# Optimization experiments

Hardware: AMD Instinct MI355X
Metric: run time of the kernel (lower is better)

The kernel has to match this reference:

```python
import jax, jax.numpy as jnp
import numpy as np

RES = 512
MAX_DEPTH = 100.0
AMBIENT = 0.3
LIGHT_STREN = 0.8
SHININESS = 16.0
EPS = 1e-8


def _unit(v):
    return v / (jnp.linalg.norm(v, axis=-1, keepdims=True) + EPS)


def setup_inputs() -> dict:
    key = jax.random.key(0)
    ks = jax.random.split(key, 8)
    B, N, M, TEX = 1, 512, 128, 512
    verts = jax.random.uniform(ks[0], (B, N, 3), minval=-1.0, maxval=1.0, dtype=jnp.float32)
    faces = jax.random.randint(ks[1], (B, M, 3), 0, N, dtype=jnp.int32)
    normals = jax.random.normal(ks[2], (B, M, 3, 3), dtype=jnp.float32)
    uvs = jax.random.uniform(ks[3], (B, M, 3, 2), dtype=jnp.float32)
    textures = jax.random.uniform(ks[4], (B, TEX, TEX, 3), dtype=jnp.float32)
    f = RES / 2.0
    K = jnp.array([[f, 0.0, RES / 2.0], [0.0, f, RES / 2.0], [0.0, 0.0, 1.0]], jnp.float32)
    Ks = jnp.broadcast_to(K, (B, 3, 3))
    RT = jnp.concatenate([jnp.eye(3, dtype=jnp.float32), jnp.array([[0.0], [0.0], [2.0]], jnp.float32)], axis=1)
    RTs = jnp.broadcast_to(RT, (B, 3, 4))
    view_dir = jax.random.normal(ks[5], (B, 3), dtype=jnp.float32)
    light_dir = jax.random.normal(ks[6], (B, 3), dtype=jnp.float32)
    return {"verts": verts, "faces": faces, "normals": normals, "uvs": uvs,
            "textures": textures, "Ks": Ks, "RTs": RTs, "view_dir": view_dir, "light_dir": light_dir}


def _render(verts, faces, normals, uvs, textures, Ks, RTs, view_dir, light_dir):
    B = verts.shape[0]
    # camera space: cam = R @ v + t
    cam = jnp.einsum('bij,bnj->bni', RTs[:, :, :3], verts) + RTs[:, None, :, 3]
    # orthographic projection to pixel coords
    x = Ks[:, None, 0, 0] * cam[..., 0] + Ks[:, None, 0, 2]
    y = Ks[:, None, 1, 1] * cam[..., 1] + Ks[:, None, 1, 2]
    xy = jnp.stack([x, y], -1)            # [B,N,2]
    z = cam[..., 2]                        # [B,N]
    gather_v = jax.vmap(lambda a, f: a[f])
    tv = gather_v(xy, faces)               # [B,M,3,2] screen-space triangle corners
    tz = gather_v(z, faces)                # [B,M,3]
    # pixel centers, row-major (p = row*RES + col)
    ii = jnp.arange(RES, dtype=jnp.float32) + 0.5
    py, px = jnp.meshgrid(ii, ii, indexing='ij')
    pix = jnp.stack([px.ravel(), py.ravel()], -1)   # [P,2]

    def edge(a, b, p):
        return (b[..., 0] - a[..., 0]) * (p[..., 1] - a[..., 1]) - (b[..., 1] - a[..., 1]) * (p[..., 0] - a[..., 0])

    v0, v1, v2 = tv[:, None, :, 0], tv[:, None, :, 1], tv[:, None, :, 2]  # [B,1,M,2]
    p = pix[None, :, None]                                               # [1,P,1,2]
    w0 = edge(v1, v2, p)                   # [B,P,M]
    w1 = edge(v2, v0, p)
    w2 = edge(v0, v1, p)
    area = w0 + w1 + w2
    inside = (((w0 >= 0) & (w1 >= 0) & (w2 >= 0)) | ((w0 <= 0) & (w1 <= 0) & (w2 <= 0))) & (jnp.abs(area) > EPS)
    inv_a = 1.0 / jnp.where(jnp.abs(area) > EPS, area, 1.0)
    zpix = (w0 * tz[:, None, :, 0] + w1 * tz[:, None, :, 1] + w2 * tz[:, None, :, 2]) * inv_a
    valid = inside & (zpix > 0)
    zc = jnp.where(valid, zpix, MAX_DEPTH)   # [B,P,M] candidate depths
    depth = jnp.min(zc, axis=-1)             # z-buffer result [B,P]
    win = jnp.argmin(zc, axis=-1)             # winning triangle per pixel [B,P]
    hit = depth < MAX_DEPTH

    # recompute barycentrics for the winning triangle only (avoids [B,P,M,3])
    gpick = jax.vmap(lambda a, i: a[i])
    tvw = gpick(tv, win)                      # [B,P,3,2]
    nw = gpick(normals, win)                  # [B,P,3,3]
    uvw = gpick(uvs, win)                     # [B,P,3,2]
    pp = pix[None]                            # [1,P,2]

    def e2(a, b):
        return (b[..., 0] - a[..., 0]) * (pp[..., 1] - a[..., 1]) - (b[..., 1] - a[..., 1]) * (pp[..., 0] - a[..., 0])

    u0 = e2(tvw[:, :, 1], tvw[:, :, 2])
    u1 = e2(tvw[:, :, 2], tvw[:, :, 0])
    u2 = e2(tvw[:, :, 0], tvw[:, :, 1])
    ar = u0 + u1 + u2
    inv2 = 1.0 / jnp.where(jnp.abs(ar) > EPS, ar, 1.0)
    bary = jnp.stack([u0, u1, u2], -1) * inv2[..., None]   # [B,P,3]
    nrm = _unit(jnp.einsum('bpk,bpkc->bpc', bary, nw))     # interpolated normal
    uv = jnp.einsum('bpk,bpkc->bpc', bary, uvw)            # interpolated uv [B,P,2]

    # bilinear texture sampling
    Ht, Wt = textures.shape[1], textures.shape[2]
    uu = jnp.clip(uv[..., 0], 0.0, 1.0) * (Wt - 1)
    vv = jnp.clip(uv[..., 1], 0.0, 1.0) * (Ht - 1)
    x0 = jnp.floor(uu).astype(jnp.int32)
    y0 = jnp.floor(vv).astype(jnp.int32)
    x1 = jnp.minimum(x0 + 1, Wt - 1)
    y1 = jnp.minimum(y0 + 1, Ht - 1)
    fx = (uu - x0.astype(jnp.float32))[..., None]
    fy = (vv - y0.astype(jnp.float32))[..., None]
    tget = jax.vmap(lambda t, a, b: t[a, b])
    col = (tget(textures, y0, x0) * (1 - fx) * (1 - fy) + tget(textures, y0, x1) * fx * (1 - fy)
           + tget(textures, y1, x0) * (1 - fx) * fy + tget(textures, y1, x1) * fx * fy)  # [B,P,3]

    # Lambert diffuse + Blinn-Phong specular
    ld = _unit(light_dir)
    vd = _unit(view_dir)
    diff = jnp.clip(jnp.einsum('bpc,bc->bp', nrm, ld), 0.0)
    h = _unit(ld + vd)
    spec = LIGHT_STREN * jnp.clip(jnp.einsum('bpc,bc->bp', nrm, h), 0.0) ** SHININESS
    shade = col * (AMBIENT + LIGHT_STREN * diff)[..., None] + spec[..., None]
    rgb = jnp.where(hit[..., None], shade, 0.0)

    depths = depth.reshape(B, RES, RES)
    rgbs = rgb.reshape(B, RES, RES, 3)
    masks = hit.reshape(B, RES, RES).astype(jnp.int32)
    return depths, rgbs, masks


def reference(verts, faces, normals, uvs, textures, Ks, RTs, view_dir, light_dir):
    return _render(verts, faces, normals, uvs, textures, Ks, RTs, view_dir, light_dir)
```

## Files before the change

kernel.cpp:

```cpp
#include <hip/hip_runtime.h>
#include <math.h>

#pragma clang fp contract(off)

#define RES         512
#define TILE        16
#define TILESX      (RES / TILE)
#define MAXF        128
#define MAX_DEPTH   100.0f
#define AMBIENT     0.3f
#define LIGHT_STREN 0.8f
#define EPSF        1e-8f
#define MARG        1.0f
#define ZGUARD      1e-3f

__global__ __launch_bounds__(256) void mesh_render_tiled(
    const float* __restrict__ verts,
    const int*   __restrict__ faces,
    const float* __restrict__ normals,
    const float* __restrict__ uvs,
    const float* __restrict__ tex,
    const float* __restrict__ Ks,
    const float* __restrict__ RTs,
    const float* __restrict__ view_dir,
    const float* __restrict__ light_dir,
    float* __restrict__ out,
    int M, int TEXW, int TEXH)
{
    __shared__ float cfd[MAXF][16];
    __shared__ int   cid[MAXF];
    __shared__ int   scnt[2][8];
    __shared__ float slit[6];

    const int tid = threadIdx.x;
    const int tx  = blockIdx.x % TILESX;
    const int ty  = blockIdx.x / TILESX;
    const float PX0 = (float)(tx * TILE) + 0.5f;
    const float PY0 = (float)(ty * TILE) + 0.5f;

    bool flag = false;
    int  bkt  = -1;
    float e0dx=0,e0dy=0,e0ax=0,e0ay=0, e1dx=0,e1dy=0,e1ax=0,e1ay=0;
    float e2dx=0,e2dy=0,e2ax=0,e2ay=0, Z0=0,Z1=0,Z2=0, MZ=0;
    unsigned long long bmask = 0;

    if (tid < MAXF) {
        if (tid < M) {
            const float r00 = RTs[0], r01 = RTs[1], r02 = RTs[2],  t0 = RTs[3];
            const float r10 = RTs[4], r11 = RTs[5], r12 = RTs[6],  t1 = RTs[7];
            const float r20 = RTs[8], r21 = RTs[9], r22 = RTs[10], t2 = RTs[11];
            const float k00 = Ks[0], k02 = Ks[2], k11 = Ks[4], k12 = Ks[5];
            float X[3], Y[3], Z[3];
            #pragma unroll
            for (int k = 0; k < 3; ++k) {
                int vi = faces[tid * 3 + k];
                float vx = verts[vi * 3 + 0];
                float vy = verts[vi * 3 + 1];
                float vz = verts[vi * 3 + 2];
                float cx = ((r00 * vx + r01 * vy) + r02 * vz) + t0;
                float cy = ((r10 * vx + r11 * vy) + r12 * vz) + t1;
                float cz = ((r20 * vx + r21 * vy) + r22 * vz) + t2;
                X[k] = k00 * cx + k02;
                Y[k] = k11 * cy + k12;
                Z[k] = cz;
            }
            e0dx = X[2]-X[1]; e0dy = Y[2]-Y[1]; e0ax = X[1]; e0ay = Y[1];
            e1dx = X[0]-X[2]; e1dy = Y[0]-Y[2]; e1ax = X[2]; e1ay = Y[2];
            e2dx = X[1]-X[0]; e2dy = Y[1]-Y[0]; e2ax = X[0]; e2ay = Y[0];
            Z0 = Z[0]; Z1 = Z[1]; Z2 = Z[2];
            MZ = fminf(fminf(Z0, Z1), Z2);

            float minX = fminf(fminf(X[0],X[1]),X[2]);
            float maxX = fmaxf(fmaxf(X[0],X[1]),X[2]);
            float minY = fminf(fminf(Y[0],Y[1]),Y[2]);
            float maxY = fmaxf(fmaxf(Y[0],Y[1]),Y[2]);
            bool bb = (minX <= PX0 + 15.0f + MARG) && (maxX >= PX0 - MARG) &&
                      (minY <= PY0 + 15.0f + MARG) && (maxY >= PY0 - MARG);

            float wA0 = e0dx*(PY0-e0ay) - e0dy*(PX0-e0ax);
            float wA1 = e1dx*(PY0-e1ay) - e1dy*(PX0-e1ax);
            float wA2 = e2dx*(PY0-e2ay) - e2dy*(PX0-e2ax);
            float area = (wA0 + wA1) + wA2;
            float amin = fminf(area, 0.0f) - MARG, amax = fmaxf(area, 0.0f) + MARG;

            float s0x = -e0dy*15.0f, s0y = e0dx*15.0f;
            float s1x = -e1dy*15.0f, s1y = e1dx*15.0f;
            float s2x = -e2dy*15.0f, s2y = e2dx*15.0f;
            float t0min = wA0 + fminf(s0x,0.f) + fminf(s0y,0.f);
            float t0max = wA0 + fmaxf(s0x,0.f) + fmaxf(s0y,0.f);
            float t1min = wA1 + fminf(s1x,0.f) + fminf(s1y,0.f);
            float t1max = wA1 + fmaxf(s1x,0.f) + fmaxf(s1y,0.f);
            float t2min = wA2 + fminf(s2x,0.f) + fminf(s2y,0.f);
            float t2max = wA2 + fmaxf(s2x,0.f) + fmaxf(s2y,0.f);
            bool ok0 = (t0max >= amin) && (t0min <= amax);
            bool ok1 = (t1max >= amin) && (t1min <= amax);
            bool ok2 = (t2max >= amin) && (t2min <= amax);
            flag = bb && ok0 && ok1 && ok2;
            if (flag) {
                int bq = (int)((MZ - 1.0f) * 4.0f);
                bkt = bq < 0 ? 0 : (bq > 7 ? 7 : bq);
            }
        }
        #pragma unroll
        for (int k = 0; k < 8; ++k) {
            unsigned long long mk = __ballot(flag && (bkt == k));
            if (bkt == k) bmask = mk;
            if ((tid & 63) == 0) scnt[tid >> 6][k] = __popcll(mk);
        }
    }
    if (tid == 128) {
        float lx = light_dir[0], ly = light_dir[1], lz = light_dir[2];
        float ll = sqrtf((lx*lx + ly*ly) + lz*lz) + 1e-8f;
        lx /= ll; ly /= ll; lz /= ll;
        float vx = view_dir[0], vy = view_dir[1], vz = view_dir[2];
        float vl = sqrtf((vx*vx + vy*vy) + vz*vz) + 1e-8f;
        vx /= vl; vy /= vl; vz /= vl;
        float hx = lx + vx, hy = ly + vy, hz = lz + vz;
        float hl = sqrtf((hx*hx + hy*hy) + hz*hz) + 1e-8f;
        slit[0] = lx; slit[1] = ly; slit[2] = lz;
        slit[3] = hx / hl; slit[4] = hy / hl; slit[5] = hz / hl;
    }
    __syncthreads();

    if (flag) {
        int wv = tid >> 6;
        int base = 0;
        for (int k = 0; k < bkt; ++k) base += scnt[0][k] + scnt[1][k];
        if (wv == 1) base += scnt[0][bkt];
        int pos = base + __popcll(bmask & ((1ull << (tid & 63)) - 1ull));
        float* dd = cfd[pos];
        dd[0]=e0dx; dd[1]=e0dy; dd[2]=e0ax; dd[3]=e0ay;
        dd[4]=e1dx; dd[5]=e1dy; dd[6]=e1ax; dd[7]=e1ay;
        dd[8]=e2dx; dd[9]=e2dy; dd[10]=e2ax; dd[11]=e2ay;
        dd[12]=Z0;  dd[13]=Z1;  dd[14]=Z2;  dd[15]=MZ - ZGUARD;
        cid[pos] = tid;
    }
    __syncthreads();
    int cnt = 0;
    #pragma unroll
    for (int k = 0; k < 8; ++k) cnt += scnt[0][k] + scnt[1][k];

    const int lx_ = tid & (TILE-1), ly_ = tid / TILE;
    const float px = PX0 + (float)lx_;
    const float py = PY0 + (float)ly_;
    const int p = (ty*TILE + ly_) * RES + (tx*TILE + lx_);

    float best = MAX_DEPTH;
    float w0s = 0.0f, w1s = 0.0f, w2s = 0.0f, invs = 1.0f;
    int winpos = -1;
    for (int i = 0; i < cnt; ++i) {
        const float4 q3 = *reinterpret_cast<const float4*>(&cfd[i][12]);
        if (__all(q3.w >= best)) continue;
        const float4 q0 = *reinterpret_cast<const float4*>(&cfd[i][0]);
        const float4 q1 = *reinterpret_cast<const float4*>(&cfd[i][4]);
        const float4 q2 = *reinterpret_cast<const float4*>(&cfd[i][8]);
        float w0 = q0.x * (py - q0.w) - q0.y * (px - q0.z);
        float w1 = q1.x * (py - q1.w) - q1.y * (px - q1.z);
        float w2 = q2.x * (py - q2.w) - q2.y * (px - q2.z);
        float area = (w0 + w1) + w2;
        float mn = fminf(fminf(w0, w1), w2);
        float mx = fmaxf(fmaxf(w0, w1), w2);
        bool nz = fabsf(area) > EPSF;
        bool inside = ((mn >= 0.0f) || (mx <= 0.0f)) && nz;
        float inva = __builtin_amdgcn_rcpf(nz ? area : 1.0f);
        float zpix = ((w0 * q3.x + w1 * q3.y) + w2 * q3.z) * inva;
        float zc = (inside && (zpix > 0.0f)) ? zpix : MAX_DEPTH;
        if (zc < best) {
            best = zc; winpos = i;
            w0s = w0; w1s = w1; w2s = w2; invs = inva;
        }
    }

    float r = 0.0f, g = 0.0f, b = 0.0f, mk = 0.0f, depth = MAX_DEPTH;
    if (winpos >= 0) {
        mk = 1.0f;
        depth = best;
        const int f = cid[winpos];
        float b0 = w0s * invs, b1 = w1s * invs, b2 = w2s * invs;

        const float* nw = normals + f * 9;
        float nx  = (b0 * nw[0] + b1 * nw[3]) + b2 * nw[6];
        float ny  = (b0 * nw[1] + b1 * nw[4]) + b2 * nw[7];
        float nzv = (b0 * nw[2] + b1 * nw[5]) + b2 * nw[8];
        float nl  = __builtin_amdgcn_sqrtf((nx*nx + ny*ny) + nzv*nzv) + 1e-8f;
        float rn  = __builtin_amdgcn_rcpf(nl);
        nx *= rn; ny *= rn; nzv *= rn;

        const float* uvp = uvs + f * 6;
        float uvx = (b0 * uvp[0] + b1 * uvp[2]) + b2 * uvp[4];
        float uvy = (b0 * uvp[1] + b1 * uvp[3]) + b2 * uvp[5];
        float uu = fminf(fmaxf(uvx, 0.0f), 1.0f) * (float)(TEXW - 1);
        float vv = fminf(fmaxf(uvy, 0.0f), 1.0f) * (float)(TEXH - 1);
        int x0 = (int)floorf(uu), y0 = (int)floorf(vv);
        int x1 = min(x0 + 1, TEXW - 1), y1 = min(y0 + 1, TEXH - 1);
        float fx = uu - (float)x0, fy = vv - (float)y0;
        const float* t00 = tex + (y0 * TEXW + x0) * 3;
        const float* t01 = tex + (y0 * TEXW + x1) * 3;
        const float* t10 = tex + (y1 * TEXW + x0) * 3;
        const float* t11 = tex + (y1 * TEXW + x1) * 3;
        float gx = 1.0f - fx, gy = 1.0f - fy;
        float cr = (((t00[0]*gx)*gy + (t01[0]*fx)*gy) + (t10[0]*gx)*fy) + (t11[0]*fx)*fy;
        float cg = (((t00[1]*gx)*gy + (t01[1]*fx)*gy) + (t10[1]*gx)*fy) + (t11[1]*fx)*fy;
        float cb = (((t00[2]*gx)*gy + (t01[2]*fx)*gy) + (t10[2]*gx)*fy) + (t11[2]*fx)*fy;

        float ldx = slit[0], ldy = slit[1], ldz = slit[2];
        float hx  = slit[3], hy  = slit[4], hz  = slit[5];
        float diff = fmaxf((nx*ldx + ny*ldy) + nzv*ldz, 0.0f);
        float sd   = fmaxf((nx*hx  + ny*hy)  + nzv*hz,  0.0f);
        float s2 = sd*sd, s4 = s2*s2, s8 = s4*s4, s16 = s8*s8;
        float spec  = LIGHT_STREN * s16;
        float scale = AMBIENT + LIGHT_STREN * diff;
        r = cr * scale + spec;
        g = cg * scale + spec;
        b = cb * scale + spec;
    }

    out[p] = depth;
    float* rgb = out + RES * RES;
    rgb[3 * p + 0] = r;
    rgb[3 * p + 1] = g;
    rgb[3 * p + 2] = b;
    out[RES * RES * 4 + p] = mk;
}

extern "C" void kernel_launch(void* const* d_in, const int* in_sizes, int n_in,
                              void* d_out, int out_size, void* d_ws, size_t ws_size,
                              hipStream_t stream) {
    const float* verts     = (const float*)d_in[0];
    const int*   faces     = (const int*)  d_in[1];
    const float* normals   = (const float*)d_in[2];
    const float* uvs       = (const float*)d_in[3];
    const float* tex       = (const float*)d_in[4];
    const float* Ks        = (const float*)d_in[5];
    const float* RTs       = (const float*)d_in[6];
    const float* view_dir  = (const float*)d_in[7];
    const float* light_dir = (const float*)d_in[8];

    int M = in_sizes[1] / 3;
    if (M > MAXF) M = MAXF;
    const int texels = in_sizes[4] / 3;
    const int TEXW = (int)(sqrt((double)texels) + 0.5);
    const int TEXH = TEXW;

    const int blocks = TILESX * TILESX;
    mesh_render_tiled<<<blocks, 256, 0, stream>>>(
        verts, faces, normals, uvs, tex, Ks, RTs, view_dir, light_dir,
        (float*)d_out, M, TEXW, TEXH);
}
```

Before: 15.68 us.

## Bin candidate triangles per 4-row wavefront strip and iterate bitmasks

Each 16x16 tile is split into four 4-row strips, one per wavefront. A conservative per-strip triangle test builds shared bitmasks, and each wave walks only the triangles set in its strip's mask using ctz iteration, skipping triangles that overlap the tile but not its own rows. Shared per-triangle storage shrinks to raw vertex coordinates, so the edge deltas are recomputed inside the loop. This adds ALU work per tested triangle and atomics during setup. The RGB store is also merged into one struct write.

Measured after the change: 16.10 us. 2.7% more time.

```diff
diff --git a/kernel.cpp b/kernel.cpp
--- a/kernel.cpp
+++ b/kernel.cpp
@@ -27,10 +27,11 @@
     float* __restrict__ out,
     int M, int TEXW, int TEXH)
 {
-    __shared__ float cfd[MAXF][16];
+    __shared__ float cfd[MAXF][12];
     __shared__ int   cid[MAXF];
     __shared__ int   scnt[2][8];
     __shared__ float slit[6];
+    __shared__ alignas(16) unsigned smstrip[4][4];
 
     const int tid = threadIdx.x;
     const int tx  = blockIdx.x % TILESX;
@@ -38,10 +39,12 @@
     const float PX0 = (float)(tx * TILE) + 0.5f;
     const float PY0 = (float)(ty * TILE) + 0.5f;
 
+    if (tid < 16) smstrip[tid >> 2][tid & 3] = 0u;
+
     bool flag = false;
+    bool sf0 = false, sf1 = false, sf2 = false, sf3 = false;
     int  bkt  = -1;
-    float e0dx=0,e0dy=0,e0ax=0,e0ay=0, e1dx=0,e1dy=0,e1ax=0,e1ay=0;
-    float e2dx=0,e2dy=0,e2ax=0,e2ay=0, Z0=0,Z1=0,Z2=0, MZ=0;
+    float X0=0,Y0=0,Z0=0, X1=0,Y1=0,Z1=0, X2=0,Y2=0,Z2=0, MZ=0;
     unsigned long long bmask = 0;
 
     if (tid < MAXF) {
@@ -64,38 +67,45 @@
                 Y[k] = k11 * cy + k12;
                 Z[k] = cz;
             }
-            e0dx = X[2]-X[1]; e0dy = Y[2]-Y[1]; e0ax = X[1]; e0ay = Y[1];
-            e1dx = X[0]-X[2]; e1dy = Y[0]-Y[2]; e1ax = X[2]; e1ay = Y[2];
-            e2dx = X[1]-X[0]; e2dy = Y[1]-Y[0]; e2ax = X[0]; e2ay = Y[0];
-            Z0 = Z[0]; Z1 = Z[1]; Z2 = Z[2];
+            X0=X[0]; Y0=Y[0]; Z0=Z[0]; X1=X[1]; Y1=Y[1]; Z1=Z[1];
+            X2=X[2]; Y2=Y[2]; Z2=Z[2];
             MZ = fminf(fminf(Z0, Z1), Z2);
 
-            float minX = fminf(fminf(X[0],X[1]),X[2]);
-            float maxX = fmaxf(fmaxf(X[0],X[1]),X[2]);
-            float minY = fminf(fminf(Y[0],Y[1]),Y[2]);
-            float maxY = fmaxf(fmaxf(Y[0],Y[1]),Y[2]);
-            bool bb = (minX <= PX0 + 15.0f + MARG) && (maxX >= PX0 - MARG) &&
-                      (minY <= PY0 + 15.0f + MARG) && (maxY >= PY0 - MARG);
-
-            float wA0 = e0dx*(PY0-e0ay) - e0dy*(PX0-e0ax);
-            float wA1 = e1dx*(PY0-e1ay) - e1dy*(PX0-e1ax);
-            float wA2 = e2dx*(PY0-e2ay) - e2dy*(PX0-e2ax);
+            float e0dx = X2-X1, e0dy = Y2-Y1;
+            float e1dx = X0-X2, e1dy = Y0-Y2;
+            float e2dx = X1-X0, e2dy = Y1-Y0;
+
+            float minX = fminf(fminf(X0,X1),X2), maxX = fmaxf(fmaxf(X0,X1),X2);
+            float minY = fminf(fminf(Y0,Y1),Y2), maxY = fmaxf(fmaxf(Y0,Y1),Y2);
+            bool bbX = (minX <= PX0 + 15.0f + MARG) && (maxX >= PX0 - MARG);
+
+            float wA0 = e0dx*(PY0-Y1) - e0dy*(PX0-X1);
+            float wA1 = e1dx*(PY0-Y2) - e1dy*(PX0-X2);
+            float wA2 = e2dx*(PY0-Y0) - e2dy*(PX0-X0);
             float area = (wA0 + wA1) + wA2;
             float amin = fminf(area, 0.0f) - MARG, amax = fmaxf(area, 0.0f) + MARG;
 
-            float s0x = -e0dy*15.0f, s0y = e0dx*15.0f;
-            float s1x = -e1dy*15.0f, s1y = e1dx*15.0f;
-            float s2x = -e2dy*15.0f, s2y = e2dx*15.0f;
-            float t0min = wA0 + fminf(s0x,0.f) + fminf(s0y,0.f);
-            float t0max = wA0 + fmaxf(s0x,0.f) + fmaxf(s0y,0.f);
-            float t1min = wA1 + fminf(s1x,0.f) + fminf(s1y,0.f);
-            float t1max = wA1 + fmaxf(s1x,0.f) + fmaxf(s1y,0.f);
-            float t2min = wA2 + fminf(s2x,0.f) + fminf(s2y,0.f);
-            float t2max = wA2 + fmaxf(s2x,0.f) + fmaxf(s2y,0.f);
-            bool ok0 = (t0max >= amin) && (t0min <= amax);
-            bool ok1 = (t1max >= amin) && (t1min <= amax);
-            bool ok2 = (t2max >= amin) && (t2min <= amax);
-            flag = bb && ok0 && ok1 && ok2;
+            float sx0 = -e0dy*15.0f, sx1 = -e1dy*15.0f, sx2 = -e2dy*15.0f;
+            float sy0 =  e0dx*3.0f,  sy1 =  e1dx*3.0f,  sy2 =  e2dx*3.0f;
+            float nx0 = fminf(sx0,0.f)+fminf(sy0,0.f), xx0 = fmaxf(sx0,0.f)+fmaxf(sy0,0.f);
+            float nx1 = fminf(sx1,0.f)+fminf(sy1,0.f), xx1 = fmaxf(sx1,0.f)+fmaxf(sy1,0.f);
+            float nx2 = fminf(sx2,0.f)+fminf(sy2,0.f), xx2 = fmaxf(sx2,0.f)+fmaxf(sy2,0.f);
+
+            bool sfl[4];
+            #pragma unroll
+            for (int w = 0; w < 4; ++w) {
+                float dy = 4.0f * (float)w;
+                float w0 = wA0 + e0dx*dy;
+                float w1 = wA1 + e1dx*dy;
+                float w2 = wA2 + e2dx*dy;
+                bool ok0 = (w0+xx0 >= amin) && (w0+nx0 <= amax);
+                bool ok1 = (w1+xx1 >= amin) && (w1+nx1 <= amax);
+                bool ok2 = (w2+xx2 >= amin) && (w2+nx2 <= amax);
+                bool bbY = (minY <= PY0+dy+3.0f+MARG) && (maxY >= PY0+dy-MARG);
+                sfl[w] = bbX && bbY && ok0 && ok1 && ok2;
+            }
+            sf0 = sfl[0]; sf1 = sfl[1]; sf2 = sfl[2]; sf3 = sfl[3];
+            flag = sf0 | sf1 | sf2 | sf3;
             if (flag) {
                 int bq = (int)((MZ - 1.0f) * 4.0f);
                 bkt = bq < 0 ? 0 : (bq > 7 ? 7 : bq);
@@ -128,46 +138,65 @@
         for (int k = 0; k < bkt; ++k) base += scnt[0][k] + scnt[1][k];
         if (wv == 1) base += scnt[0][bkt];
         int pos = base + __popcll(bmask & ((1ull << (tid & 63)) - 1ull));
-        float* dd = cfd[pos];
-        dd[0]=e0dx; dd[1]=e0dy; dd[2]=e0ax; dd[3]=e0ay;
-        dd[4]=e1dx; dd[5]=e1dy; dd[6]=e1ax; dd[7]=e1ay;
-        dd[8]=e2dx; dd[9]=e2dy; dd[10]=e2ax; dd[11]=e2ay;
-        dd[12]=Z0;  dd[13]=Z1;  dd[14]=Z2;  dd[15]=MZ - ZGUARD;
+        float4* dd = (float4*)cfd[pos];
+        dd[0] = make_float4(X0, Y0, Z0, MZ - ZGUARD);
+        dd[1] = make_float4(X1, Y1, Z1, 0.0f);
+        dd[2] = make_float4(X2, Y2, Z2, 0.0f);
         cid[pos] = tid;
+        unsigned bit = 1u << (pos & 31);
+        int word = pos >> 5;
+        if (sf0) atomicOr(&smstrip[0][word], bit);
+        if (sf1) atomicOr(&smstrip[1][word], bit);
+        if (sf2) atomicOr(&smstrip[2][word], bit);
+        if (sf3) atomicOr(&smstrip[3][word], bit);
     }
     __syncthreads();
-    int cnt = 0;
-    #pragma unroll
-    for (int k = 0; k < 8; ++k) cnt += scnt[0][k] + scnt[1][k];
 
     const int lx_ = tid & (TILE-1), ly_ = tid / TILE;
+    const int wv  = tid >> 6;
     const float px = PX0 + (float)lx_;
     const float py = PY0 + (float)ly_;
     const int p = (ty*TILE + ly_) * RES + (tx*TILE + lx_);
 
+    const uint4 mm = *(const uint4*)smstrip[wv];
+    unsigned long long m0 =
+        ((unsigned long long)(unsigned)__builtin_amdgcn_readfirstlane(mm.y) << 32) |
+         (unsigned long long)(unsigned)__builtin_amdgcn_readfirstlane(mm.x);
+    unsigned long long m1 =
+        ((unsigned long long)(unsigned)__builtin_amdgcn_readfirstlane(mm.w) << 32) |
+         (unsigned long long)(unsigned)__builtin_amdgcn_readfirstlane(mm.z);
+
     float best = MAX_DEPTH;
     float w0s = 0.0f, w1s = 0.0f, w2s = 0.0f, invs = 1.0f;
     int winpos = -1;
-    for (int i = 0; i < cnt; ++i) {
-        const float4 q3 = *reinterpret_cast<const float4*>(&cfd[i][12]);
-        if (__all(q3.w >= best)) continue;
-        const float4 q0 = *reinterpret_cast<const float4*>(&cfd[i][0]);
-        const float4 q1 = *reinterpret_cast<const float4*>(&cfd[i][4]);
-        const float4 q2 = *reinterpret_cast<const float4*>(&cfd[i][8]);
-        float w0 = q0.x * (py - q0.w) - q0.y * (px - q0.z);
-        float w1 = q1.x * (py - q1.w) - q1.y * (px - q1.z);
-        float w2 = q2.x * (py - q2.w) - q2.y * (px - q2.z);
-        float area = (w0 + w1) + w2;
-        float mn = fminf(fminf(w0, w1), w2);
-        float mx = fmaxf(fmaxf(w0, w1), w2);
-        bool nz = fabsf(area) > EPSF;
-        bool inside = ((mn >= 0.0f) || (mx <= 0.0f)) && nz;
-        float inva = __builtin_amdgcn_rcpf(nz ? area : 1.0f);
-        float zpix = ((w0 * q3.x + w1 * q3.y) + w2 * q3.z) * inva;
-        float zc = (inside && (zpix > 0.0f)) ? zpix : MAX_DEPTH;
-        if (zc < best) {
-            best = zc; winpos = i;
-            w0s = w0; w1s = w1; w2s = w2; invs = inva;
+
+    #pragma unroll 1
+    for (int half = 0; half < 2; ++half) {
+        unsigned long long m = half ? m1 : m0;
+        int off = half ? 64 : 0;
+        while (m) {
+            int i = off + (int)__builtin_ctzll(m);
+            m &= m - 1;
+            float mzg = cfd[i][3];
+            if (__all(mzg >= best)) continue;
+            const float4 q0 = *reinterpret_cast<const float4*>(&cfd[i][0]);
+            const float4 q1 = *reinterpret_cast<const float4*>(&cfd[i][4]);
+            const float4 q2 = *reinterpret_cast<const float4*>(&cfd[i][8]);
+            float w0 = (q2.x - q1.x) * (py - q1.y) - (q2.y - q1.y) * (px - q1.x);
+            float w1 = (q0.x - q2.x) * (py - q2.y) - (q0.y - q2.y) * (px - q2.x);
+            float w2 = (q1.x - q0.x) * (py - q0.y) - (q1.y - q0.y) * (px - q0.x);
+            float area = (w0 + w1) + w2;
+            float mn = fminf(fminf(w0, w1), w2);
+            float mx = fmaxf(fmaxf(w0, w1), w2);
+            bool nz = fabsf(area) > EPSF;
+            bool inside = ((mn >= 0.0f) || (mx <= 0.0f)) && nz;
+            float inva = __builtin_amdgcn_rcpf(nz ? area : 1.0f);
+            float zpix = ((w0 * q0.z + w1 * q1.z) + w2 * q2.z) * inva;
+            float zc = (inside && (zpix > 0.0f)) ? zpix : MAX_DEPTH;
+            if (zc < best) {
+                best = zc; winpos = i;
+                w0s = w0; w1s = w1; w2s = w2; invs = inva;
+            }
         }
     }
 
@@ -216,10 +245,8 @@
     }
 
     out[p] = depth;
-    float* rgb = out + RES * RES;
-    rgb[3 * p + 0] = r;
-    rgb[3 * p + 1] = g;
-    rgb[3 * p + 2] = b;
+    struct F3 { float x, y, z; };
+    ((F3*)(out + RES * RES))[p] = F3{r, g, b};
     out[RES * RES * 4 + p] = mk;
 }
 
```

## Compact per-face shared data, add bucket-level early exit, vectorize global loads

Applied to the files above, without the earlier changes.

Stores triangle vertices in shared memory as 40 bytes per face instead of 64 edge-precomputed floats, and recomputes edge deltas in the raster loop. The loop walks the depth buckets and exits once a bucket's lower depth bound cannot beat any lane's current best. Normals, UVs and texture texels are read with packed 16-byte and 8-byte loads: both x-neighbour texels come from one contiguous row read, with a select at the right edge. RGB output is written as a 12-byte struct. This cuts LDS traffic and global load instructions, at the cost of extra ALU work per triangle test.

Measured after the change: 16.21 us. 1.03x slower.

```diff
diff --git a/kernel.cpp b/kernel.cpp
--- a/kernel.cpp
+++ b/kernel.cpp
@@ -13,6 +13,11 @@
 #define EPSF        1e-8f
 #define MARG        1.0f
 #define ZGUARD      1e-3f
+
+struct __attribute__((packed, aligned(4))) PF4 { float a, b, c, d; };
+struct __attribute__((packed, aligned(4))) PF2 { float a, b; };
+static __device__ __forceinline__ PF4 ld4(const float* p) { PF4 v; __builtin_memcpy(&v, p, 16); return v; }
+static __device__ __forceinline__ PF2 ld2(const float* p) { PF2 v; __builtin_memcpy(&v, p, 8); return v; }
 
 __global__ __launch_bounds__(256) void mesh_render_tiled(
     const float* __restrict__ verts,
@@ -27,10 +32,12 @@
     float* __restrict__ out,
     int M, int TEXW, int TEXH)
 {
-    __shared__ float cfd[MAXF][16];
-    __shared__ int   cid[MAXF];
-    __shared__ int   scnt[2][8];
-    __shared__ float slit[6];
+    __shared__ float4 smA[MAXF];
+    __shared__ float4 smB[MAXF];
+    __shared__ float2 smC[MAXF];
+    __shared__ int    cid[MAXF];
+    __shared__ int    scnt[2][8];
+    __shared__ float  slit[6];
 
     const int tid = threadIdx.x;
     const int tx  = blockIdx.x % TILESX;
@@ -40,8 +47,7 @@
 
     bool flag = false;
     int  bkt  = -1;
-    float e0dx=0,e0dy=0,e0ax=0,e0ay=0, e1dx=0,e1dy=0,e1ax=0,e1ay=0;
-    float e2dx=0,e2dy=0,e2ax=0,e2ay=0, Z0=0,Z1=0,Z2=0, MZ=0;
+    float X0=0,Y0=0,Z0=0, X1=0,Y1=0,Z1=0, X2=0,Y2=0,Z2=0, MZ=0;
     unsigned long long bmask = 0;
 
     if (tid < MAXF) {
@@ -64,22 +70,22 @@
                 Y[k] = k11 * cy + k12;
                 Z[k] = cz;
             }
-            e0dx = X[2]-X[1]; e0dy = Y[2]-Y[1]; e0ax = X[1]; e0ay = Y[1];
-            e1dx = X[0]-X[2]; e1dy = Y[0]-Y[2]; e1ax = X[2]; e1ay = Y[2];
-            e2dx = X[1]-X[0]; e2dy = Y[1]-Y[0]; e2ax = X[0]; e2ay = Y[0];
-            Z0 = Z[0]; Z1 = Z[1]; Z2 = Z[2];
+            X0=X[0]; Y0=Y[0]; Z0=Z[0]; X1=X[1]; Y1=Y[1]; Z1=Z[1];
+            X2=X[2]; Y2=Y[2]; Z2=Z[2];
             MZ = fminf(fminf(Z0, Z1), Z2);
 
-            float minX = fminf(fminf(X[0],X[1]),X[2]);
-            float maxX = fmaxf(fmaxf(X[0],X[1]),X[2]);
-            float minY = fminf(fminf(Y[0],Y[1]),Y[2]);
-            float maxY = fmaxf(fmaxf(Y[0],Y[1]),Y[2]);
+            float e0dx = X2-X1, e0dy = Y2-Y1;
+            float e1dx = X0-X2, e1dy = Y0-Y2;
+            float e2dx = X1-X0, e2dy = Y1-Y0;
+
+            float minX = fminf(fminf(X0,X1),X2), maxX = fmaxf(fmaxf(X0,X1),X2);
+            float minY = fminf(fminf(Y0,Y1),Y2), maxY = fmaxf(fmaxf(Y0,Y1),Y2);
             bool bb = (minX <= PX0 + 15.0f + MARG) && (maxX >= PX0 - MARG) &&
                       (minY <= PY0 + 15.0f + MARG) && (maxY >= PY0 - MARG);
 
-            float wA0 = e0dx*(PY0-e0ay) - e0dy*(PX0-e0ax);
-            float wA1 = e1dx*(PY0-e1ay) - e1dy*(PX0-e1ax);
-            float wA2 = e2dx*(PY0-e2ay) - e2dy*(PX0-e2ax);
+            float wA0 = e0dx*(PY0-Y1) - e0dy*(PX0-X1);
+            float wA1 = e1dx*(PY0-Y2) - e1dy*(PX0-X2);
+            float wA2 = e2dx*(PY0-Y0) - e2dy*(PX0-X0);
             float area = (wA0 + wA1) + wA2;
             float amin = fminf(area, 0.0f) - MARG, amax = fmaxf(area, 0.0f) + MARG;
 
@@ -128,17 +134,19 @@
         for (int k = 0; k < bkt; ++k) base += scnt[0][k] + scnt[1][k];
         if (wv == 1) base += scnt[0][bkt];
         int pos = base + __popcll(bmask & ((1ull << (tid & 63)) - 1ull));
-        float* dd = cfd[pos];
-        dd[0]=e0dx; dd[1]=e0dy; dd[2]=e0ax; dd[3]=e0ay;
-        dd[4]=e1dx; dd[5]=e1dy; dd[6]=e1ax; dd[7]=e1ay;
-        dd[8]=e2dx; dd[9]=e2dy; dd[10]=e2ax; dd[11]=e2ay;
-        dd[12]=Z0;  dd[13]=Z1;  dd[14]=Z2;  dd[15]=MZ - ZGUARD;
+        smA[pos] = make_float4(X0, Y0, X1, Y1);
+        smB[pos] = make_float4(X2, Y2, Z0, Z1);
+        smC[pos] = make_float2(MZ - ZGUARD, Z2);
         cid[pos] = tid;
     }
     __syncthreads();
-    int cnt = 0;
-    #pragma unroll
-    for (int k = 0; k < 8; ++k) cnt += scnt[0][k] + scnt[1][k];
+
+    int bend[8];
+    {
+        int acc = 0;
+        #pragma unroll
+        for (int k = 0; k < 8; ++k) { acc += scnt[0][k] + scnt[1][k]; bend[k] = acc; }
+    }
 
     const int lx_ = tid & (TILE-1), ly_ = tid / TILE;
     const float px = PX0 + (float)lx_;
@@ -148,26 +156,34 @@
     float best = MAX_DEPTH;
     float w0s = 0.0f, w1s = 0.0f, w2s = 0.0f, invs = 1.0f;
     int winpos = -1;
-    for (int i = 0; i < cnt; ++i) {
-        const float4 q3 = *reinterpret_cast<const float4*>(&cfd[i][12]);
-        if (__all(q3.w >= best)) continue;
-        const float4 q0 = *reinterpret_cast<const float4*>(&cfd[i][0]);
-        const float4 q1 = *reinterpret_cast<const float4*>(&cfd[i][4]);
-        const float4 q2 = *reinterpret_cast<const float4*>(&cfd[i][8]);
-        float w0 = q0.x * (py - q0.w) - q0.y * (px - q0.z);
-        float w1 = q1.x * (py - q1.w) - q1.y * (px - q1.z);
-        float w2 = q2.x * (py - q2.w) - q2.y * (px - q2.z);
-        float area = (w0 + w1) + w2;
-        float mn = fminf(fminf(w0, w1), w2);
-        float mx = fmaxf(fmaxf(w0, w1), w2);
-        bool nz = fabsf(area) > EPSF;
-        bool inside = ((mn >= 0.0f) || (mx <= 0.0f)) && nz;
-        float inva = __builtin_amdgcn_rcpf(nz ? area : 1.0f);
-        float zpix = ((w0 * q3.x + w1 * q3.y) + w2 * q3.z) * inva;
-        float zc = (inside && (zpix > 0.0f)) ? zpix : MAX_DEPTH;
-        if (zc < best) {
-            best = zc; winpos = i;
-            w0s = w0; w1s = w1; w2s = w2; invs = inva;
+
+    int i = 0;
+    #pragma unroll 1
+    for (int k = 0; k < 8; ++k) {
+        const int e = bend[k];
+        if (i >= e) continue;
+        float lbk = (1.0f + 0.25f * (float)k) - ZGUARD;
+        if (__all(lbk >= best)) break;
+        for (; i < e; ++i) {
+            const float2 c = smC[i];
+            if (__all(c.x >= best)) continue;
+            const float4 A = smA[i];
+            const float4 B = smB[i];
+            float w0 = (B.x - A.z) * (py - A.w) - (B.y - A.w) * (px - A.z);
+            float w1 = (A.x - B.x) * (py - B.y) - (A.y - B.y) * (px - B.x);
+            float w2 = (A.z - A.x) * (py - A.y) - (A.w - A.y) * (px - A.x);
+            float area = (w0 + w1) + w2;
+            float mn = fminf(fminf(w0, w1), w2);
+            float mx = fmaxf(fmaxf(w0, w1), w2);
+            bool nz = fabsf(area) > EPSF;
+            bool inside = ((mn >= 0.0f) || (mx <= 0.0f)) && nz;
+            float inva = __builtin_amdgcn_rcpf(nz ? area : 1.0f);
+            float zpix = ((w0 * B.z + w1 * B.w) + w2 * c.y) * inva;
+            float zc = (inside && (zpix > 0.0f)) ? zpix : MAX_DEPTH;
+            if (zc < best) {
+                best = zc; winpos = i;
+                w0s = w0; w1s = w1; w2s = w2; invs = inva;
+            }
         }
     }
 
@@ -179,29 +195,39 @@
         float b0 = w0s * invs, b1 = w1s * invs, b2 = w2s * invs;
 
         const float* nw = normals + f * 9;
-        float nx  = (b0 * nw[0] + b1 * nw[3]) + b2 * nw[6];
-        float ny  = (b0 * nw[1] + b1 * nw[4]) + b2 * nw[7];
-        float nzv = (b0 * nw[2] + b1 * nw[5]) + b2 * nw[8];
+        PF4 n0 = ld4(nw); PF4 n1 = ld4(nw + 4); float n8 = nw[8];
+        float nx  = (b0 * n0.a + b1 * n0.d) + b2 * n1.c;
+        float ny  = (b0 * n0.b + b1 * n1.a) + b2 * n1.d;
+        float nzv = (b0 * n0.c + b1 * n1.b) + b2 * n8;
         float nl  = __builtin_amdgcn_sqrtf((nx*nx + ny*ny) + nzv*nzv) + 1e-8f;
         float rn  = __builtin_amdgcn_rcpf(nl);
         nx *= rn; ny *= rn; nzv *= rn;
 
         const float* uvp = uvs + f * 6;
-        float uvx = (b0 * uvp[0] + b1 * uvp[2]) + b2 * uvp[4];
-        float uvy = (b0 * uvp[1] + b1 * uvp[3]) + b2 * uvp[5];
+        PF4 u0 = ld4(uvp); PF2 u1 = ld2(uvp + 4);
+        float uvx = (b0 * u0.a + b1 * u0.c) + b2 * u1.a;
+        float uvy = (b0 * u0.b + b1 * u0.d) + b2 * u1.b;
         float uu = fminf(fmaxf(uvx, 0.0f), 1.0f) * (float)(TEXW - 1);
         float vv = fminf(fmaxf(uvy, 0.0f), 1.0f) * (float)(TEXH - 1);
         int x0 = (int)floorf(uu), y0 = (int)floorf(vv);
-        int x1 = min(x0 + 1, TEXW - 1), y1 = min(y0 + 1, TEXH - 1);
+        int y1 = min(y0 + 1, TEXH - 1);
         float fx = uu - (float)x0, fy = vv - (float)y0;
-        const float* t00 = tex + (y0 * TEXW + x0) * 3;
-        const float* t01 = tex + (y0 * TEXW + x1) * 3;
-        const float* t10 = tex + (y1 * TEXW + x0) * 3;
-        const float* t11 = tex + (y1 * TEXW + x1) * 3;
+
+        int xb = min(x0, TEXW - 2);
+        bool xe = (x0 == TEXW - 1);
+        const float* r0 = tex + (y0 * TEXW + xb) * 3;
+        const float* r1 = tex + (y1 * TEXW + xb) * 3;
+        PF4 a0 = ld4(r0); PF2 a1 = ld2(r0 + 4);
+        PF4 c0 = ld4(r1); PF2 c1 = ld2(r1 + 4);
+        float t00r = xe ? a0.d : a0.a, t00g = xe ? a1.a : a0.b, t00b = xe ? a1.b : a0.c;
+        float t01r = a0.d,             t01g = a1.a,             t01b = a1.b;
+        float t10r = xe ? c0.d : c0.a, t10g = xe ? c1.a : c0.b, t10b = xe ? c1.b : c0.c;
+        float t11r = c0.d,             t11g = c1.a,             t11b = c1.b;
+
         float gx = 1.0f - fx, gy = 1.0f - fy;
-        float cr = (((t00[0]*gx)*gy + (t01[0]*fx)*gy) + (t10[0]*gx)*fy) + (t11[0]*fx)*fy;
-        float cg = (((t00[1]*gx)*gy + (t01[1]*fx)*gy) + (t10[1]*gx)*fy) + (t11[1]*fx)*fy;
-        float cb = (((t00[2]*gx)*gy + (t01[2]*fx)*gy) + (t10[2]*gx)*fy) + (t11[2]*fx)*fy;
+        float cr = (((t00r*gx)*gy + (t01r*fx)*gy) + (t10r*gx)*fy) + (t11r*fx)*fy;
+        float cg = (((t00g*gx)*gy + (t01g*fx)*gy) + (t10g*gx)*fy) + (t11g*fx)*fy;
+        float cb = (((t00b*gx)*gy + (t01b*fx)*gy) + (t10b*gx)*fy) + (t11b*fx)*fy;
 
         float ldx = slit[0], ldy = slit[1], ldz = slit[2];
         float hx  = slit[3], hy  = slit[4], hz  = slit[5];
@@ -216,10 +242,8 @@
     }
 
     out[p] = depth;
-    float* rgb = out + RES * RES;
-    rgb[3 * p + 0] = r;
-    rgb[3 * p + 1] = g;
-    rgb[3 * p + 2] = b;
+    struct F3 { float x, y, z; };
+    ((F3*)(out + RES * RES))[p] = F3{r, g, b};
     out[RES * RES * 4 + p] = mk;
 }
 
```
